# Optimization experiments

Measured on AMD Instinct MI355X. Metric: run time of the kernel, lower is better.

Reference implementation:

```python
import jax, jax.numpy as jnp
import numpy as np
from jax import lax

B, H, W, C = 16, 56, 56, 256
NH = 8
KD = C // NH  # key/head dim = 32
FF = 1024
EPS = 1e-6
SCALE = KD ** -0.5


def _layernorm(x, g, b):
    m = jnp.mean(x, axis=-1, keepdims=True)
    v = jnp.mean(jnp.square(x - m), axis=-1, keepdims=True)
    return (x - m) * lax.rsqrt(v + EPS) * g + b


def _dwconv(x, w, b):
    # x: (B,H,W,Cd), w: (kh,kw,1,Cd) depthwise (groups = Cd), stride 1, SAME padding
    return lax.conv_general_dilated(
        x, w, window_strides=(1, 1), padding='SAME',
        dimension_numbers=('NHWC', 'HWIO', 'NHWC'),
        feature_group_count=x.shape[-1]) + b


def setup_inputs() -> dict:
    key = jax.random.key(0)
    ks = jax.random.split(key, 20)
    r = lambda i, shape, s=0.02: jax.random.normal(ks[i], shape, jnp.float32) * s
    return {
        'x': jax.random.normal(ks[0], (B, H, W, C), jnp.float32),
        'mask_h': jax.random.normal(ks[1], (NH, H, H), jnp.float32),
        'mask_w': jax.random.normal(ks[2], (NH, W, W), jnp.float32),
        # pos: DWConv2d(C, 3, 1, 1)
        'pos_w': r(3, (3, 3, 1, C)), 'pos_b': jnp.zeros((C,), jnp.float32),
        # retention layer norm
        'ln1_g': jnp.ones((C,), jnp.float32), 'ln1_b': jnp.zeros((C,), jnp.float32),
        # MaSA projections (stored as (in, out) so y = x @ W + b)
        'q_w': r(4, (C, C)), 'q_b': jnp.zeros((C,), jnp.float32),
        'k_w': r(5, (C, C)), 'k_b': jnp.zeros((C,), jnp.float32),
        'v_w': r(6, (C, C)), 'v_b': jnp.zeros((C,), jnp.float32),
        # lepe: DWConv2d(C, 5, 1, 2)
        'lepe_w': r(7, (5, 5, 1, C)), 'lepe_b': jnp.zeros((C,), jnp.float32),
        'out_w': r(8, (C, C)), 'out_b': jnp.zeros((C,), jnp.float32),
        # final layer norm
        'ln2_g': jnp.ones((C,), jnp.float32), 'ln2_b': jnp.zeros((C,), jnp.float32),
        # FFN
        'fc1_w': r(9, (C, FF)), 'fc1_b': jnp.zeros((FF,), jnp.float32),
        'fc2_w': r(10, (FF, C)), 'fc2_b': jnp.zeros((C,), jnp.float32),
    }


def _masa(x, mask_h, mask_w, q_w, q_b, k_w, k_b, v_w, v_b, lepe_w, lepe_b, out_w, out_b):
    b, h, w, _ = x.shape
    q = x @ q_w + q_b
    k = (x @ k_w + k_b) * SCALE
    v = x @ v_w + v_b
    lepe = _dwconv(v, lepe_w, lepe_b)
    qh = q.reshape(b, h, w, NH, KD)
    kh = k.reshape(b, h, w, NH, KD)
    vh = v.reshape(b, h, w, NH, KD)
    # width-axis retention: scores (b, h, NH, w, w), mask_w broadcasts as (NH, w, w)
    attn_w = jax.nn.softmax(jnp.einsum('bhqnd,bhknd->bhnqk', qh, kh) + mask_w, axis=-1)
    vw = jnp.einsum('bhnqk,bhknd->bhnqd', attn_w, vh)  # (b, h, NH, w, KD)
    # height-axis retention: scores (b, w, NH, h, h), mask_h broadcasts as (NH, h, h)
    attn_h = jax.nn.softmax(jnp.einsum('bqwnd,bkwnd->bwnqk', qh, kh) + mask_h, axis=-1)
    out = jnp.einsum('bwnqk,bknwd->bqwnd', attn_h, vw)  # (b, h, w, NH, KD)
    out = out.reshape(b, h, w, NH * KD) + lepe
    return out @ out_w + out_b


def reference(x, mask_h, mask_w, pos_w, pos_b, ln1_g, ln1_b,
              q_w, q_b, k_w, k_b, v_w, v_b, lepe_w, lepe_b, out_w, out_b,
              ln2_g, ln2_b, fc1_w, fc1_b, fc2_w, fc2_b):
    # RetBlock (retention='whole', no layerscale, no dropout / drop_path)
    x = x + _dwconv(x, pos_w, pos_b)
    x = x + _masa(_layernorm(x, ln1_g, ln1_b), mask_h, mask_w,
                  q_w, q_b, k_w, k_b, v_w, v_b, lepe_w, lepe_b, out_w, out_b)
    y = _layernorm(x, ln2_g, ln2_b)
    y = jax.nn.gelu(y @ fc1_w + fc1_b, approximate=False) @ fc2_w + fc2_b
    return x + y
```

## Files before the change

### kernel.cpp

```cpp
#include <hip/hip_runtime.h>
#include <hip/hip_bf16.h>
#include <math.h>
#include <stdint.h>

typedef __bf16 bf16;
typedef __bf16 bf16x8 __attribute__((ext_vector_type(8)));
typedef __bf16 bf16x4 __attribute__((ext_vector_type(4)));
typedef float f32x4 __attribute__((ext_vector_type(4)));

#define AS1 __attribute__((address_space(1)))
#define AS3 __attribute__((address_space(3)))

#define NPIX (16*56*56)
#define CH 256
#define SCALE_K 0.17677669529663687f

__device__ __forceinline__ float gelu_fast(float vv) {
    float t = vv * (-2.30220781f + -0.10294330f * vv * vv);
    float e = __builtin_amdgcn_exp2f(t);
    return vv * __builtin_amdgcn_rcpf(1.0f + e);
}

__global__ __launch_bounds__(256) void pre_kernel(
    const float* __restrict__ x, const float* __restrict__ pos_w,
    const float* __restrict__ pos_b, const float* __restrict__ ln1_g,
    const float* __restrict__ ln1_b, float* __restrict__ x1,
    bf16* __restrict__ tln,
    const float* __restrict__ q_w, const float* __restrict__ k_w,
    const float* __restrict__ v_w, const float* __restrict__ out_w,
    const float* __restrict__ fc1_w, const float* __restrict__ fc2_w,
    const float* __restrict__ qb, const float* __restrict__ kb,
    const float* __restrict__ vb,
    bf16* __restrict__ wt_qkv, bf16* __restrict__ wt_out,
    bf16* __restrict__ wt_fc1, bf16* __restrict__ wt_fc2,
    float* __restrict__ qkvb)
{
    if (blockIdx.x >= 12544) {
        int idx = (blockIdx.x - 12544) * 256 + threadIdx.x;
        if (idx < 262144) {
            int w = idx >> 16;
            int j = idx & 65535;
            int n = j >> 8, k = j & 255;
            const float* src = (w == 0) ? q_w : (w == 1) ? k_w : (w == 2) ? v_w : out_w;
            float scale = (w == 1) ? SCALE_K : 1.0f;
            bf16* dst = (w < 3) ? (wt_qkv + w * 65536) : wt_out;
            dst[j] = (bf16)(src[k * 256 + n] * scale);
        } else if (idx < 524288) {
            int j = idx - 262144;
            int n = j >> 8, k = j & 255;
            wt_fc1[j] = (bf16)(fc1_w[k * 1024 + n]);
        } else if (idx < 786432) {
            int j = idx - 524288;
            int n = j >> 10, k = j & 1023;
            wt_fc2[j] = (bf16)(fc2_w[k * 256 + n]);
        } else if (idx < 787200) {
            int i = idx - 786432;
            qkvb[i] = (i < 256) ? qb[i] : (i < 512) ? kb[i - 256] * SCALE_K : vb[i - 512];
        }
        return;
    }
    const int wave = threadIdx.x >> 6, lane = threadIdx.x & 63;
    const long pix = (long)blockIdx.x * 4 + wave;
    const int ww = (int)(pix % 56);
    const int hh = (int)((pix / 56) % 56);
    const int b  = (int)(pix / 3136);
    const int c  = lane * 4;
    float4 acc = ((const float4*)(pos_b + c))[0];
    float4 xin = ((const float4*)(x + pix * 256 + c))[0];
    acc.x += xin.x; acc.y += xin.y; acc.z += xin.z; acc.w += xin.w;
    #pragma unroll
    for (int dh = 0; dh < 3; ++dh) {
        int h2 = hh + dh - 1;
        if (h2 < 0 || h2 >= 56) continue;
        #pragma unroll
        for (int dw = 0; dw < 3; ++dw) {
            int w2 = ww + dw - 1;
            if (w2 < 0 || w2 >= 56) continue;
            float4 xv = ((const float4*)(x + (((long)(b * 56 + h2)) * 56 + w2) * 256 + c))[0];
            float4 wv = ((const float4*)(pos_w + (dh * 3 + dw) * 256 + c))[0];
            acc.x += xv.x * wv.x; acc.y += xv.y * wv.y;
            acc.z += xv.z * wv.z; acc.w += xv.w * wv.w;
        }
    }
    ((float4*)(x1 + pix * 256 + c))[0] = acc;
    float s  = acc.x + acc.y + acc.z + acc.w;
    float q2 = acc.x * acc.x + acc.y * acc.y + acc.z * acc.z + acc.w * acc.w;
    #pragma unroll
    for (int o = 32; o; o >>= 1) {
        s  += __shfl_xor(s,  o, 64);
        q2 += __shfl_xor(q2, o, 64);
    }
    float mean = s * (1.0f / 256.0f);
    float var  = q2 * (1.0f / 256.0f) - mean * mean;
    float rs   = rsqrtf(var + 1e-6f);
    float4 gv = ((const float4*)ln1_g)[lane];
    float4 bv = ((const float4*)ln1_b)[lane];
    bf16* o4 = tln + pix * 256 + c;
    o4[0] = (bf16)((acc.x - mean) * rs * gv.x + bv.x);
    o4[1] = (bf16)((acc.y - mean) * rs * gv.y + bv.y);
    o4[2] = (bf16)((acc.z - mean) * rs * gv.z + bv.z);
    o4[3] = (bf16)((acc.w - mean) * rs * gv.w + bv.w);
}

__global__ __launch_bounds__(256) void lepe_kernel(
    const bf16* __restrict__ vpl, const float* __restrict__ w,
    const float* __restrict__ bias, bf16* __restrict__ out)
{
    long idx = (long)blockIdx.x * 256 + threadIdx.x;
    int c8 = (int)(idx & 31);
    long pix = idx >> 5;
    int ww = (int)(pix % 56);
    int hh = (int)((pix / 56) % 56);
    int b  = (int)(pix / 3136);
    int c  = c8 * 8;
    float acc[8];
    #pragma unroll
    for (int j = 0; j < 8; ++j) acc[j] = bias[c + j];
    #pragma unroll
    for (int dh = 0; dh < 5; ++dh) {
        int h2 = hh + dh - 2;
        if (h2 < 0 || h2 >= 56) continue;
        #pragma unroll
        for (int dw = 0; dw < 5; ++dw) {
            int w2 = ww + dw - 2;
            if (w2 < 0 || w2 >= 56) continue;
            bf16x8 vv = *(const bf16x8*)(vpl + (((long)(b * 56 + h2)) * 56 + w2) * 256 + c);
            const float4* wp = (const float4*)(w + (dh * 5 + dw) * 256 + c);
            float4 w0 = wp[0], w1 = wp[1];
            acc[0] += (float)vv[0] * w0.x; acc[1] += (float)vv[1] * w0.y;
            acc[2] += (float)vv[2] * w0.z; acc[3] += (float)vv[3] * w0.w;
            acc[4] += (float)vv[4] * w1.x; acc[5] += (float)vv[5] * w1.y;
            acc[6] += (float)vv[6] * w1.z; acc[7] += (float)vv[7] * w1.w;
        }
    }
    bf16* o = out + pix * 256 + c;
    #pragma unroll
    for (int j = 0; j < 8; ++j) o[j] = (bf16)acc[j];
}

template<bool WIDTH>
__global__ __launch_bounds__(256) void attn_mfma_kernel(
    const bf16* __restrict__ qp, const bf16* __restrict__ kp,
    const bf16* __restrict__ vsrc, const float* __restrict__ mask,
    const bf16* __restrict__ lepe, bf16* __restrict__ outp)
{
    __shared__ bf16 VtAll[4][32][72];
    __shared__ bf16 PlAll[4][16][72];
    const int tid = threadIdx.x;
    const int wave = tid >> 6, lane = tid & 63;
    const int g = lane >> 4, ql = lane & 15;
    const int n  = blockIdx.x / 224;
    const int s  = (blockIdx.x % 224) * 4 + wave;
    const int b  = s / 56, rc = s % 56;
    bf16 (*Vt)[72] = VtAll[wave];
    bf16 (*Pl)[72] = PlAll[wave];
    const long basePix = WIDTH ? ((long)(b * 56 + rc)) * 56 : (long)b * 3136 + rc;
    const long pixStride = WIDTH ? 1 : 56;
    const long stride = pixStride * 256;
    const bf16* qb = qp + basePix * 256 + n * 32;
    const bf16* kb = kp + basePix * 256 + n * 32;
    const bf16* vbp = vsrc + basePix * 256 + n * 32;

    #pragma unroll
    for (int it = 0; it < 2; ++it) {
        int idx = it * 64 + lane;
        if (idx < 112) {
            int pp = idx >> 2, chunk = idx & 3;
            int pos0 = pp * 2;
            bf16x8 v0 = *(const bf16x8*)(vbp + (long)pos0 * stride + chunk * 8);
            bf16x8 v1 = *(const bf16x8*)(vbp + (long)(pos0 + 1) * stride + chunk * 8);
            int colb = pos0 ^ (chunk << 3);
            #pragma unroll
            for (int j = 0; j < 8; ++j) {
                union { bf16 h[2]; unsigned int u; } pk;
                pk.h[0] = v0[j]; pk.h[1] = v1[j];
                *(unsigned int*)&Vt[chunk * 8 + j][colb] = pk.u;
            }
        }
    }
    if (lane < 32) {
        int d = lane;
        int colb = 56 ^ ((d >> 3) << 3);
        *(float4*)&Vt[d][colb] = (float4){0.f, 0.f, 0.f, 0.f};
    }

    bf16x8 qf[4], kf[4];
    #pragma unroll
    for (int t4 = 0; t4 < 4; ++t4) {
        int row = ql + 16 * t4; if (row > 55) row = 55;
        qf[t4] = *(const bf16x8*)(qb + (long)row * stride + 8 * g);
        kf[t4] = *(const bf16x8*)(kb + (long)row * stride + 8 * g);
    }

    f32x4 sA[4][4];
    __builtin_amdgcn_s_setprio(1);
    #pragma unroll
    for (int qt = 0; qt < 4; ++qt)
        #pragma unroll
        for (int kt = 0; kt < 4; ++kt)
            sA[qt][kt] = __builtin_amdgcn_mfma_f32_16x16x32_bf16(
                kf[kt], qf[qt], (f32x4){0.f, 0.f, 0.f, 0.f}, 0, 0, 0);
    __builtin_amdgcn_s_setprio(0);

    const float* mrow = mask + n * 3136;
    #pragma unroll
    for (int qt = 0; qt < 4; ++qt) {
        int qm = ql + 16 * qt; if (qm > 55) qm = 55;
        #pragma unroll
        for (int kt = 0; kt < 4; ++kt) {
            if (kt == 3 && g >= 2) {
                sA[qt][3][0] = -3.0e38f; sA[qt][3][1] = -3.0e38f;
                sA[qt][3][2] = -3.0e38f; sA[qt][3][3] = -3.0e38f;
            } else {
                float4 mv = *(const float4*)(mrow + qm * 56 + kt * 16 + 4 * g);
                sA[qt][kt][0] += mv.x; sA[qt][kt][1] += mv.y;
                sA[qt][kt][2] += mv.z; sA[qt][kt][3] += mv.w;
            }
        }
    }

    #pragma unroll
    for (int qt = 0; qt < 4; ++qt) {
        float m = -3.0e38f;
        #pragma unroll
        for (int kt = 0; kt < 4; ++kt)
            #pragma unroll
            for (int r = 0; r < 4; ++r) m = fmaxf(m, sA[qt][kt][r]);
        m = fmaxf(m, __shfl_xor(m, 16, 64));
        m = fmaxf(m, __shfl_xor(m, 32, 64));
        float p[4][4];
        float sum = 0.f;
        #pragma unroll
        for (int kt = 0; kt < 4; ++kt)
            #pragma unroll
            for (int r = 0; r < 4; ++r) {
                float e = exp2f((sA[qt][kt][r] - m) * 1.4426950408889634f);
                p[kt][r] = e; sum += e;
            }
        sum += __shfl_xor(sum, 16, 64);
        sum += __shfl_xor(sum, 32, 64);
        float rinv = 1.0f / sum;
        #pragma unroll
        for (int kt = 0; kt < 4; ++kt) {
            bf16x4 w;
            #pragma unroll
            for (int r = 0; r < 4; ++r) w[r] = (bf16)(p[kt][r] * rinv);
            *(bf16x4*)&Pl[ql][kt * 16 + 4 * g] = w;
        }
        #pragma unroll
        for (int nt = 0; nt < 2; ++nt) {
            f32x4 o = {0.f, 0.f, 0.f, 0.f};
            __builtin_amdgcn_s_setprio(1);
            #pragma unroll
            for (int ks = 0; ks < 2; ++ks) {
                bf16x8 af = *(const bf16x8*)&Pl[ql][ks * 32 + 8 * g];
                int vrow = ql + 16 * nt;
                int vcol = (ks * 32 + 8 * g) ^ ((vrow >> 3) << 3);
                bf16x8 bv = *(const bf16x8*)&Vt[vrow][vcol];
                o = __builtin_amdgcn_mfma_f32_16x16x32_bf16(af, bv, o, 0, 0, 0);
            }
            __builtin_amdgcn_s_setprio(0);
            if (!(qt == 3 && g >= 2)) {
                #pragma unroll
                for (int r = 0; r < 4; ++r) {
                    int q = 16 * qt + 4 * g + r;
                    long addr = (basePix + (long)q * pixStride) * 256 + n * 32 + nt * 16 + ql;
                    float vv = o[r];
                    if (!WIDTH) vv += (float)lepe[addr];
                    outp[addr] = (bf16)vv;
                }
            }
        }
    }
}

template<bool GELU, bool RESID, bool OUT_BF16, bool QKV3>
__global__ __launch_bounds__(512) void gemm_kernel(
    const bf16* __restrict__ A, const bf16* __restrict__ Wt,
    const float* __restrict__ bias, const float* __restrict__ resid,
    void* __restrict__ Cout, int M, int N, int K)
{
    __shared__ bf16 As[256 * 64];
    __shared__ bf16 Bs[128 * 64];
    const int t = threadIdx.x;
    const int wave = t >> 6, lane = t & 63;
    const int nTilesN = N >> 7;
    const int q8 = gridDim.x >> 3;
    const int o = ((int)blockIdx.x & 7) * q8 + ((int)blockIdx.x >> 3);
    const int tm = o / nTilesN, tn = o % nTilesN;
    const long m0 = (long)tm * 256, n0 = (long)tn * 128;
    const int waveM = (wave >> 1) * 64, waveN = (wave & 1) * 64;
    f32x4 acc[4][4] = {};

    for (int k0 = 0; k0 < K; k0 += 64) {
        #pragma unroll
        for (int i = 0; i < 4; ++i) {
            int c = i * 512 + t;
            int r = c >> 3, cc = (c & 7) * 8;
            const bf16* ga = A + (m0 + r) * (long)K + k0 + cc;
            __builtin_amdgcn_global_load_lds(
                (const AS1 void*)ga, (AS3 void*)(As + c * 8), 16, 0, 0);
        }
        #pragma unroll
        for (int i = 0; i < 2; ++i) {
            int c = i * 512 + t;
            int r = c >> 3, cc = (c & 7) * 8;
            const bf16* gb = Wt + (n0 + r) * (long)K + k0 + cc;
            __builtin_amdgcn_global_load_lds(
                (const AS1 void*)gb, (AS3 void*)(Bs + c * 8), 16, 0, 0);
        }
        __syncthreads();
        #pragma unroll
        for (int kk = 0; kk < 2; ++kk) {
            bf16x8 af[4], bfr[4];
            const int krow = kk * 32 + (lane >> 4) * 8;
            #pragma unroll
            for (int fm = 0; fm < 4; ++fm)
                af[fm] = *(const bf16x8*)&As[(waveM + fm * 16 + (lane & 15)) * 64 + krow];
            #pragma unroll
            for (int fn = 0; fn < 4; ++fn)
                bfr[fn] = *(const bf16x8*)&Bs[(waveN + fn * 16 + (lane & 15)) * 64 + krow];
            #pragma unroll
            for (int fm = 0; fm < 4; ++fm)
                #pragma unroll
                for (int fn = 0; fn < 4; ++fn)
                    acc[fm][fn] = __builtin_amdgcn_mfma_f32_16x16x32_bf16(
                        af[fm], bfr[fn], acc[fm][fn], 0, 0, 0);
        }
        __syncthreads();
    }

    #pragma unroll
    for (int fm = 0; fm < 4; ++fm) {
        #pragma unroll
        for (int r = 0; r < 4; ++r) {
            const long m = m0 + waveM + fm * 16 + (lane >> 4) * 4 + r;
            #pragma unroll
            for (int fn = 0; fn < 4; ++fn) {
                const long n = n0 + waveN + fn * 16 + (lane & 15);
                float vv = acc[fm][fn][r] + bias[n];
                if (GELU)  vv = gelu_fast(vv);
                if (RESID) vv += resid[m * N + n];
                if (QKV3) {
                    long pl = n >> 8;
                    ((bf16*)Cout)[pl * (long)NPIX * 256 + m * 256 + (n & 255)] = (bf16)vv;
                } else if (OUT_BF16) {
                    ((bf16*)Cout)[m * N + n] = (bf16)vv;
                } else {
                    ((float*)Cout)[m * N + n] = vv;
                }
            }
        }
    }
}

__global__ __launch_bounds__(512) void outln_kernel(
    const bf16* __restrict__ A, const bf16* __restrict__ Wt,
    const float* __restrict__ bias, const float* __restrict__ resid,
    const float* __restrict__ g2, const float* __restrict__ b2,
    float* __restrict__ x2out, bf16* __restrict__ uout)
{
    __shared__ bf16 As[128 * 64];
    __shared__ bf16 Bs[256 * 64];
    const int t = threadIdx.x;
    const int wave = t >> 6, lane = t & 63;
    const int g = lane >> 4, ql = lane & 15;
    const int q8 = gridDim.x >> 3;
    const int o = ((int)blockIdx.x & 7) * q8 + ((int)blockIdx.x >> 3);
    const long m0 = (long)o * 128;
    const int waveM = wave * 16;
    f32x4 acc[16] = {};

    for (int k0 = 0; k0 < 256; k0 += 64) {
        #pragma unroll
        for (int i = 0; i < 2; ++i) {
            int c = i * 512 + t;
            int r = c >> 3, cc = (c & 7) * 8;
            const bf16* ga = A + (m0 + r) * 256 + k0 + cc;
            __builtin_amdgcn_global_load_lds(
                (const AS1 void*)ga, (AS3 void*)(As + c * 8), 16, 0, 0);
        }
        #pragma unroll
        for (int i = 0; i < 4; ++i) {
            int c = i * 512 + t;
            int r = c >> 3, cc = (c & 7) * 8;
            const bf16* gb = Wt + r * 256 + k0 + cc;
            __builtin_amdgcn_global_load_lds(
                (const AS1 void*)gb, (AS3 void*)(Bs + c * 8), 16, 0, 0);
        }
        __syncthreads();
        #pragma unroll
        for (int kk = 0; kk < 2; ++kk) {
            const int krow = kk * 32 + g * 8;
            bf16x8 af = *(const bf16x8*)&As[(waveM + ql) * 64 + krow];
            #pragma unroll
            for (int fn = 0; fn < 16; ++fn) {
                bf16x8 bv = *(const bf16x8*)&Bs[(fn * 16 + ql) * 64 + krow];
                acc[fn] = __builtin_amdgcn_mfma_f32_16x16x32_bf16(af, bv, acc[fn], 0, 0, 0);
            }
        }
        __syncthreads();
    }

    float rsum[4] = {}, rsq[4] = {};
    #pragma unroll
    for (int fn = 0; fn < 16; ++fn) {
        const int n = fn * 16 + ql;
        const float bn = bias[n];
        #pragma unroll
        for (int r = 0; r < 4; ++r) {
            const long m = m0 + waveM + g * 4 + r;
            float v = acc[fn][r] + bn + resid[m * 256 + n];
            acc[fn][r] = v;
            rsum[r] += v; rsq[r] += v * v;
        }
    }
    #pragma unroll
    for (int r = 0; r < 4; ++r) {
        float s = rsum[r], q = rsq[r];
        #pragma unroll
        for (int off = 8; off; off >>= 1) {
            s += __shfl_xor(s, off, 64);
            q += __shfl_xor(q, off, 64);
        }
        float mean = s * (1.0f / 256.0f);
        float var  = q * (1.0f / 256.0f) - mean * mean;
        rsum[r] = mean;
        rsq[r]  = rsqrtf(var + 1e-6f);
    }
    #pragma unroll
    for (int fn = 0; fn < 16; ++fn) {
        const int n = fn * 16 + ql;
        const float gn = g2[n], bn2 = b2[n];
        #pragma unroll
        for (int r = 0; r < 4; ++r) {
            const long m = m0 + waveM + g * 4 + r;
            float v = acc[fn][r];
            x2out[m * 256 + n] = v;
            uout[m * 256 + n] = (bf16)((v - rsum[r]) * rsq[r] * gn + bn2);
        }
    }
}

extern "C" void kernel_launch(void* const* d_in, const int* in_sizes, int n_in,
                              void* d_out, int out_size, void* d_ws, size_t ws_size,
                              hipStream_t stream)
{
    (void)in_sizes; (void)n_in; (void)out_size; (void)ws_size;
    const float* x      = (const float*)d_in[0];
    const float* mask_h = (const float*)d_in[1];
    const float* mask_w = (const float*)d_in[2];
    const float* pos_w  = (const float*)d_in[3];
    const float* pos_b  = (const float*)d_in[4];
    const float* ln1_g  = (const float*)d_in[5];
    const float* ln1_b  = (const float*)d_in[6];
    const float* q_w    = (const float*)d_in[7];
    const float* q_b    = (const float*)d_in[8];
    const float* k_w    = (const float*)d_in[9];
    const float* k_b    = (const float*)d_in[10];
    const float* v_w    = (const float*)d_in[11];
    const float* v_b    = (const float*)d_in[12];
    const float* lepe_w = (const float*)d_in[13];
    const float* lepe_b = (const float*)d_in[14];
    const float* out_w  = (const float*)d_in[15];
    const float* out_b  = (const float*)d_in[16];
    const float* ln2_g  = (const float*)d_in[17];
    const float* ln2_b  = (const float*)d_in[18];
    const float* fc1_w  = (const float*)d_in[19];
    const float* fc1_b  = (const float*)d_in[20];
    const float* fc2_w  = (const float*)d_in[21];
    const float* fc2_b  = (const float*)d_in[22];

    char* ws = (char*)d_ws;
    size_t off = 0;
    auto alloc = [&](size_t bytes) -> void* {
        void* p = ws + off;
        off += (bytes + 255) & ~(size_t)255;
        return p;
    };
    const int M = NPIX;
    float* x1     = (float*)alloc((size_t)M * 256 * 4);
    bf16*  tln    = (bf16*) alloc((size_t)M * 256 * 2);
    bf16*  qkv3   = (bf16*) alloc((size_t)M * 768 * 2);
    bf16*  lepeb  = (bf16*) alloc((size_t)M * 256 * 2);
    bf16*  vwb    = (bf16*) alloc((size_t)M * 256 * 2);
    bf16*  obuf   = (bf16*) alloc((size_t)M * 256 * 2);
    bf16*  wt_qkv = (bf16*) alloc((size_t)768 * 256 * 2);
    bf16*  wt_out = (bf16*) alloc((size_t)256 * 256 * 2);
    bf16*  wt_fc1 = (bf16*) alloc((size_t)1024 * 256 * 2);
    bf16*  wt_fc2 = (bf16*) alloc((size_t)256 * 1024 * 2);
    float* qkvb   = (float*)alloc(768 * 4);
    bf16*  qpl    = qkv3;
    bf16*  kpl    = qkv3 + (size_t)M * 256;
    bf16*  vpl    = qkv3 + (size_t)M * 512;
    bf16*  h1     = tln;
    float* outf   = (float*)d_out;

    pre_kernel<<<12544 + 3075, 256, 0, stream>>>(
        x, pos_w, pos_b, ln1_g, ln1_b, x1, tln,
        q_w, k_w, v_w, out_w, fc1_w, fc2_w, q_b, k_b, v_b,
        wt_qkv, wt_out, wt_fc1, wt_fc2, qkvb);

    gemm_kernel<false, false, true, true><<<196 * 6, 512, 0, stream>>>(
        tln, wt_qkv, qkvb, nullptr, qkv3, M, 768, 256);
    lepe_kernel<<<6272, 256, 0, stream>>>(vpl, lepe_w, lepe_b, lepeb);
    attn_mfma_kernel<true><<<1792, 256, 0, stream>>>(qpl, kpl, vpl, mask_w, nullptr, vwb);
    attn_mfma_kernel<false><<<1792, 256, 0, stream>>>(qpl, kpl, vwb, mask_h, lepeb, obuf);
    outln_kernel<<<392, 512, 0, stream>>>(
        obuf, wt_out, out_b, x1, ln2_g, ln2_b, outf, lepeb);
    gemm_kernel<true, false, true, false><<<196 * 8, 512, 0, stream>>>(
        lepeb, wt_fc1, fc1_b, nullptr, h1, M, 1024, 256);
    gemm_kernel<false, true, false, false><<<196 * 2, 512, 0, stream>>>(
        h1, wt_fc2, fc2_b, outf, outf, M, 256, 1024);
}
```

Before: 400.8 us.

## Store residual x1 in bf16 and merge lepe conv into width-attention launch

The residual stream x1 written by the pre kernel is now stored in bf16 instead of fp32, which halves its write traffic and the later read in the out-projection/LayerNorm kernel. The depthwise lepe convolution is folded into the width-axis attention kernel as extra blocks, so the two independent tasks share one launch and can overlap on the GPU. The bf16 residual adds rounding error to a path that was previously kept in full precision. The fused kernel's register and shared-memory use is set by the attention body, which may lower occupancy for the conv blocks.

```diff
diff --git a/kernel.cpp b/kernel.cpp
--- a/kernel.cpp
+++ b/kernel.cpp
@@ -24,7 +24,7 @@
 __global__ __launch_bounds__(256) void pre_kernel(
     const float* __restrict__ x, const float* __restrict__ pos_w,
     const float* __restrict__ pos_b, const float* __restrict__ ln1_g,
-    const float* __restrict__ ln1_b, float* __restrict__ x1,
+    const float* __restrict__ ln1_b, bf16* __restrict__ x1,
     bf16* __restrict__ tln,
     const float* __restrict__ q_w, const float* __restrict__ k_w,
     const float* __restrict__ v_w, const float* __restrict__ out_w,
@@ -82,7 +82,9 @@
             acc.z += xv.z * wv.z; acc.w += xv.w * wv.w;
         }
     }
-    ((float4*)(x1 + pix * 256 + c))[0] = acc;
+    bf16* x1o = x1 + pix * 256 + c;
+    x1o[0] = (bf16)acc.x; x1o[1] = (bf16)acc.y;
+    x1o[2] = (bf16)acc.z; x1o[3] = (bf16)acc.w;
     float s  = acc.x + acc.y + acc.z + acc.w;
     float q2 = acc.x * acc.x + acc.y * acc.y + acc.z * acc.z + acc.w * acc.w;
     #pragma unroll
@@ -102,44 +104,9 @@
     o4[3] = (bf16)((acc.w - mean) * rs * gv.w + bv.w);
 }
 
-__global__ __launch_bounds__(256) void lepe_kernel(
-    const bf16* __restrict__ vpl, const float* __restrict__ w,
-    const float* __restrict__ bias, bf16* __restrict__ out)
-{
-    long idx = (long)blockIdx.x * 256 + threadIdx.x;
-    int c8 = (int)(idx & 31);
-    long pix = idx >> 5;
-    int ww = (int)(pix % 56);
-    int hh = (int)((pix / 56) % 56);
-    int b  = (int)(pix / 3136);
-    int c  = c8 * 8;
-    float acc[8];
-    #pragma unroll
-    for (int j = 0; j < 8; ++j) acc[j] = bias[c + j];
-    #pragma unroll
-    for (int dh = 0; dh < 5; ++dh) {
-        int h2 = hh + dh - 2;
-        if (h2 < 0 || h2 >= 56) continue;
-        #pragma unroll
-        for (int dw = 0; dw < 5; ++dw) {
-            int w2 = ww + dw - 2;
-            if (w2 < 0 || w2 >= 56) continue;
-            bf16x8 vv = *(const bf16x8*)(vpl + (((long)(b * 56 + h2)) * 56 + w2) * 256 + c);
-            const float4* wp = (const float4*)(w + (dh * 5 + dw) * 256 + c);
-            float4 w0 = wp[0], w1 = wp[1];
-            acc[0] += (float)vv[0] * w0.x; acc[1] += (float)vv[1] * w0.y;
-            acc[2] += (float)vv[2] * w0.z; acc[3] += (float)vv[3] * w0.w;
-            acc[4] += (float)vv[4] * w1.x; acc[5] += (float)vv[5] * w1.y;
-            acc[6] += (float)vv[6] * w1.z; acc[7] += (float)vv[7] * w1.w;
-        }
-    }
-    bf16* o = out + pix * 256 + c;
-    #pragma unroll
-    for (int j = 0; j < 8; ++j) o[j] = (bf16)acc[j];
-}
-
 template<bool WIDTH>
-__global__ __launch_bounds__(256) void attn_mfma_kernel(
+__device__ __forceinline__ void attn_body(
+    int task,
     const bf16* __restrict__ qp, const bf16* __restrict__ kp,
     const bf16* __restrict__ vsrc, const float* __restrict__ mask,
     const bf16* __restrict__ lepe, bf16* __restrict__ outp)
@@ -149,8 +116,8 @@
     const int tid = threadIdx.x;
     const int wave = tid >> 6, lane = tid & 63;
     const int g = lane >> 4, ql = lane & 15;
-    const int n  = blockIdx.x / 224;
-    const int s  = (blockIdx.x % 224) * 4 + wave;
+    const int n  = task / 224;
+    const int s  = (task % 224) * 4 + wave;
     const int b  = s / 56, rc = s % 56;
     bf16 (*Vt)[72] = VtAll[wave];
     bf16 (*Pl)[72] = PlAll[wave];
@@ -272,6 +239,57 @@
             }
         }
     }
+}
+
+__global__ __launch_bounds__(256) void attnw_lepe_kernel(
+    const bf16* __restrict__ qp, const bf16* __restrict__ kp,
+    const bf16* __restrict__ vpl, const float* __restrict__ mask_w,
+    bf16* __restrict__ vwb,
+    const float* __restrict__ lw, const float* __restrict__ lb,
+    bf16* __restrict__ lepeb)
+{
+    if (blockIdx.x < 1792) {
+        attn_body<true>(blockIdx.x, qp, kp, vpl, mask_w, nullptr, vwb);
+        return;
+    }
+    long idx = (long)(blockIdx.x - 1792) * 256 + threadIdx.x;
+    int c8 = (int)(idx & 31);
+    long pix = idx >> 5;
+    int ww = (int)(pix % 56);
+    int hh = (int)((pix / 56) % 56);
+    int b  = (int)(pix / 3136);
+    int c  = c8 * 8;
+    float acc[8];
+    #pragma unroll
+    for (int j = 0; j < 8; ++j) acc[j] = lb[c + j];
+    #pragma unroll
+    for (int dh = 0; dh < 5; ++dh) {
+        int h2 = hh + dh - 2;
+        if (h2 < 0 || h2 >= 56) continue;
+        #pragma unroll
+        for (int dw = 0; dw < 5; ++dw) {
+            int w2 = ww + dw - 2;
+            if (w2 < 0 || w2 >= 56) continue;
+            bf16x8 vv = *(const bf16x8*)(vpl + (((long)(b * 56 + h2)) * 56 + w2) * 256 + c);
+            const float4* wp = (const float4*)(lw + (dh * 5 + dw) * 256 + c);
+            float4 w0 = wp[0], w1 = wp[1];
+            acc[0] += (float)vv[0] * w0.x; acc[1] += (float)vv[1] * w0.y;
+            acc[2] += (float)vv[2] * w0.z; acc[3] += (float)vv[3] * w0.w;
+            acc[4] += (float)vv[4] * w1.x; acc[5] += (float)vv[5] * w1.y;
+            acc[6] += (float)vv[6] * w1.z; acc[7] += (float)vv[7] * w1.w;
+        }
+    }
+    bf16* o = lepeb + pix * 256 + c;
+    #pragma unroll
+    for (int j = 0; j < 8; ++j) o[j] = (bf16)acc[j];
+}
+
+__global__ __launch_bounds__(256) void attnh_kernel(
+    const bf16* __restrict__ qp, const bf16* __restrict__ kp,
+    const bf16* __restrict__ vwb, const float* __restrict__ mask_h,
+    const bf16* __restrict__ lepeb, bf16* __restrict__ obuf)
+{
+    attn_body<false>(blockIdx.x, qp, kp, vwb, mask_h, lepeb, obuf);
 }
 
 template<bool GELU, bool RESID, bool OUT_BF16, bool QKV3>
@@ -356,7 +374,7 @@
 
 __global__ __launch_bounds__(512) void outln_kernel(
     const bf16* __restrict__ A, const bf16* __restrict__ Wt,
-    const float* __restrict__ bias, const float* __restrict__ resid,
+    const float* __restrict__ bias, const bf16* __restrict__ resid,
     const float* __restrict__ g2, const float* __restrict__ b2,
     float* __restrict__ x2out, bf16* __restrict__ uout)
 {
@@ -410,7 +428,7 @@
         #pragma unroll
         for (int r = 0; r < 4; ++r) {
             const long m = m0 + waveM + g * 4 + r;
-            float v = acc[fn][r] + bn + resid[m * 256 + n];
+            float v = acc[fn][r] + bn + (float)resid[m * 256 + n];
             acc[fn][r] = v;
             rsum[r] += v; rsq[r] += v * v;
         }
@@ -479,7 +497,7 @@
         return p;
     };
     const int M = NPIX;
-    float* x1     = (float*)alloc((size_t)M * 256 * 4);
+    bf16*  x1     = (bf16*) alloc((size_t)M * 256 * 2);
     bf16*  tln    = (bf16*) alloc((size_t)M * 256 * 2);
     bf16*  qkv3   = (bf16*) alloc((size_t)M * 768 * 2);
     bf16*  lepeb  = (bf16*) alloc((size_t)M * 256 * 2);
@@ -503,9 +521,9 @@
 
     gemm_kernel<false, false, true, true><<<196 * 6, 512, 0, stream>>>(
         tln, wt_qkv, qkvb, nullptr, qkv3, M, 768, 256);
-    lepe_kernel<<<6272, 256, 0, stream>>>(vpl, lepe_w, lepe_b, lepeb);
-    attn_mfma_kernel<true><<<1792, 256, 0, stream>>>(qpl, kpl, vpl, mask_w, nullptr, vwb);
-    attn_mfma_kernel<false><<<1792, 256, 0, stream>>>(qpl, kpl, vwb, mask_h, lepeb, obuf);
+    attnw_lepe_kernel<<<1792 + 6272, 256, 0, stream>>>(
+        qpl, kpl, vpl, mask_w, vwb, lepe_w, lepe_b, lepeb);
+    attnh_kernel<<<1792, 256, 0, stream>>>(qpl, kpl, vwb, mask_h, lepeb, obuf);
     outln_kernel<<<392, 512, 0, stream>>>(
         obuf, wt_out, out_b, x1, ln2_g, ln2_b, outf, lepeb);
     gemm_kernel<true, false, true, false><<<196 * 8, 512, 0, stream>>>(
```

New measurement: 434.4 us. 8.4% more time.
